# Kernel tuning notes

Hardware: AMD Instinct MI355X
Metric: run time of the kernel (lower is better)

## Reference

```python
import jax, jax.numpy as jnp
import numpy as np

N = 50000      # nodes
E = 800000     # edges (avg degree 16)
F_IN = 64      # node_feature_space
H = 64         # hidden_dim
G = 16         # graphs in batch
BN_EPS = 1e-5


def setup_inputs() -> dict:
    key = jax.random.key(0)
    ks = jax.random.split(key, 8)
    x = jax.random.normal(ks[0], (N, F_IN), jnp.float32)
    edge_index = jax.random.randint(ks[1], (2, E), 0, N, dtype=jnp.int64)
    batch = jnp.sort(jax.random.randint(ks[2], (N,), 0, G, dtype=jnp.int64))
    init = lambda k, shp, fan: jax.random.normal(k, shp, jnp.float32) / np.float32(np.sqrt(fan))
    params = dict(
        W1_0=init(ks[3], (F_IN, H), F_IN), b1_0=jnp.zeros((H,), jnp.float32),
        W2_0=init(ks[4], (H, H), H),       b2_0=jnp.zeros((H,), jnp.float32),
        g_0=jnp.ones((H,), jnp.float32),   be_0=jnp.zeros((H,), jnp.float32),
        W1_1=init(ks[5], (H, H), H),       b1_1=jnp.zeros((H,), jnp.float32),
        W2_1=init(ks[6], (H, H), H),       b2_1=jnp.zeros((H,), jnp.float32),
        g_1=jnp.ones((H,), jnp.float32),   be_1=jnp.zeros((H,), jnp.float32),
    )
    return dict(x=x, edge_index=edge_index, batch=batch, **params)


def _gin_layer(x, src, dst, W1, b1, W2, b2, g, be):
    # GINConv (eps=0): h_i = MLP(x_i + sum_{j->i} x_j)
    agg = jax.ops.segment_sum(x[src], dst, num_segments=N)   # [N, d]
    h = x + agg
    h = jnp.maximum(h @ W1 + b1, 0.0) @ W2 + b2              # Linear-ReLU-Linear
    # BatchNorm1d (training-mode batch stats, biased variance as in torch)
    mu = h.mean(axis=0)
    var = h.var(axis=0)
    h = (h - mu) * jax.lax.rsqrt(var + BN_EPS) * g + be
    return jnp.maximum(h, 0.0)                               # ReLU


def reference(x, edge_index, batch,
              W1_0, b1_0, W2_0, b2_0, g_0, be_0,
              W1_1, b1_1, W2_1, b2_1, g_1, be_1):
    src, dst = edge_index[0], edge_index[1]
    x = _gin_layer(x, src, dst, W1_0, b1_0, W2_0, b2_0, g_0, be_0)
    x = _gin_layer(x, src, dst, W1_1, b1_1, W2_1, b2_1, g_1, be_1)
    # global_mean_pool over graph ids
    cnt = jax.ops.segment_sum(jnp.ones((N,), x.dtype), batch, num_segments=G)
    sums = jax.ops.segment_sum(x, batch, num_segments=G)
    h_graph = sums / jnp.maximum(cnt, 1.0)[:, None]
    return (x, h_graph)
```

## Files before the change

kernel.cpp:

```cpp
#include <hip/hip_runtime.h>
#include <hip/hip_bf16.h>


constexpr int NN = 50000;
constexpr int NE = 800000;
constexpr int HD = 64;
constexpr int NG = 16;
constexpr float BN_EPS = 1e-5f;
constexpr int ROWCAP = 64;
constexpr int NPART = 8;
constexpr int PSZ = 6250;
constexpr int PBLK = (PSZ + 3) / 4;

__global__ __launch_bounds__(256)
void prep_kernel(const float* __restrict__ x, __hip_bfloat16* __restrict__ xb,
                 int* __restrict__ cnt, float* __restrict__ stats0,
                 float* __restrict__ stats1, float* __restrict__ psums) {
    int i4 = blockIdx.x * 256 + threadIdx.x;
    if (i4 < NN) cnt[i4] = 0;
    if (blockIdx.x == 0) {
        if (threadIdx.x < 128) stats0[threadIdx.x] = 0.f;
        else stats1[threadIdx.x - 128] = 0.f;
    } else if (blockIdx.x == 1) {
        *(float4*)(psums + threadIdx.x * 4) = make_float4(0.f, 0.f, 0.f, 0.f);
    }
    if (i4 >= NN * HD / 4) return;
    float4 v = *(const float4*)(x + (size_t)i4 * 4);
    union { ushort4 u; __hip_bfloat16 b[4]; } p;
    p.b[0] = __float2bfloat16(v.x);
    p.b[1] = __float2bfloat16(v.y);
    p.b[2] = __float2bfloat16(v.z);
    p.b[3] = __float2bfloat16(v.w);
    *(ushort4*)((unsigned short*)xb + (size_t)i4 * 4) = p.u;
}

__global__ __launch_bounds__(256)
void scatter_kernel(const int* __restrict__ ei, int* __restrict__ cnt,
                    unsigned short* __restrict__ csr) {
    int p = blockIdx.x & 7;
    int chunk = blockIdx.x >> 3;
    int e4 = (chunk * 256 + threadIdx.x) * 4;
    if (e4 >= NE) return;
    int4 s = *(const int4*)(ei + e4);
    int4 d = *(const int4*)(ei + NE + e4);
    int lo = p * PSZ, hi = lo + PSZ;
    int slot;
    if (d.x >= lo && d.x < hi) {
        slot = atomicAdd(&cnt[d.x], 1);
        if (slot < ROWCAP) csr[(d.x << 6) + slot] = (unsigned short)s.x;
    }
    if (d.y >= lo && d.y < hi) {
        slot = atomicAdd(&cnt[d.y], 1);
        if (slot < ROWCAP) csr[(d.y << 6) + slot] = (unsigned short)s.y;
    }
    if (d.z >= lo && d.z < hi) {
        slot = atomicAdd(&cnt[d.z], 1);
        if (slot < ROWCAP) csr[(d.z << 6) + slot] = (unsigned short)s.z;
    }
    if (d.w >= lo && d.w < hi) {
        slot = atomicAdd(&cnt[d.w], 1);
        if (slot < ROWCAP) csr[(d.w << 6) + slot] = (unsigned short)s.w;
    }
}

template <int MODE>
__global__ __launch_bounds__(256)
void agg_kernel(const float* __restrict__ xin, const __hip_bfloat16* __restrict__ xg,
                const int* __restrict__ cnt, const unsigned short* __restrict__ csr,
                const float* __restrict__ stats_prev, const float* __restrict__ gp,
                const float* __restrict__ bep, float* __restrict__ h) {
    int lr = ((blockIdx.x >> 3) << 2) + (threadIdx.x >> 6);
    if (lr >= PSZ) return;
    int row = (blockIdx.x & 7) * PSZ + lr;
    int lane = threadIdx.x & 63;
    int s4 = (lane & 15) * 4;
    int g = lane >> 4;

    float4 sc4 = make_float4(1.f, 1.f, 1.f, 1.f);
    float4 off4 = make_float4(0.f, 0.f, 0.f, 0.f);
    if (MODE == 1) {
        const float inv = 1.f / (float)NN;
        float4 sm = *(const float4*)(stats_prev + s4);
        float4 sq = *(const float4*)(stats_prev + 64 + s4);
        float4 gg = *(const float4*)(gp + s4);
        float4 bb = *(const float4*)(bep + s4);
        float mu, var;
        mu = sm.x * inv; var = sq.x * inv - mu * mu;
        sc4.x = gg.x * rsqrtf(var + BN_EPS); off4.x = bb.x - mu * sc4.x;
        mu = sm.y * inv; var = sq.y * inv - mu * mu;
        sc4.y = gg.y * rsqrtf(var + BN_EPS); off4.y = bb.y - mu * sc4.y;
        mu = sm.z * inv; var = sq.z * inv - mu * mu;
        sc4.z = gg.z * rsqrtf(var + BN_EPS); off4.z = bb.z - mu * sc4.z;
        mu = sm.w * inv; var = sq.w * inv - mu * mu;
        sc4.w = gg.w * rsqrtf(var + BN_EPS); off4.w = bb.w - mu * sc4.w;
    }

    int m = min(cnt[row], ROWCAP);
    int ids = (int)csr[((size_t)row << 6) + lane];
    const unsigned short* xgp = (const unsigned short*)xg;

    float4 accA = make_float4(0.f, 0.f, 0.f, 0.f);
    float4 accB = make_float4(0.f, 0.f, 0.f, 0.f);
    if (g == 0) {
        float4 sv = *(const float4*)(xin + (size_t)row * HD + s4);
        if (MODE == 1) {
            accA.x = fmaxf(fmaf(sv.x, sc4.x, off4.x), 0.f);
            accA.y = fmaxf(fmaf(sv.y, sc4.y, off4.y), 0.f);
            accA.z = fmaxf(fmaf(sv.z, sc4.z, off4.z), 0.f);
            accA.w = fmaxf(fmaf(sv.w, sc4.w, off4.w), 0.f);
        } else {
            accA = sv;
        }
    }

#define ACC_U2(ACC, U)                                                        \
    {                                                                         \
        float v0 = __uint_as_float((U).x << 16);                              \
        float v1 = __uint_as_float((U).x & 0xffff0000u);                      \
        float v2 = __uint_as_float((U).y << 16);                              \
        float v3 = __uint_as_float((U).y & 0xffff0000u);                      \
        if (MODE == 1) {                                                      \
            ACC.x += fmaxf(fmaf(v0, sc4.x, off4.x), 0.f);                     \
            ACC.y += fmaxf(fmaf(v1, sc4.y, off4.y), 0.f);                     \
            ACC.z += fmaxf(fmaf(v2, sc4.z, off4.z), 0.f);                     \
            ACC.w += fmaxf(fmaf(v3, sc4.w, off4.w), 0.f);                     \
        } else {                                                              \
            ACC.x += v0; ACC.y += v1; ACC.z += v2; ACC.w += v3;               \
        }                                                                     \
    }

    int j = 0;
    for (; j + 8 <= m; j += 8) {
        int nb0 = __shfl(ids, j + g);
        int nb1 = __shfl(ids, j + 4 + g);
        uint2 u0 = *(const uint2*)(xgp + ((size_t)nb0 << 6) + s4);
        uint2 u1 = *(const uint2*)(xgp + ((size_t)nb1 << 6) + s4);
        ACC_U2(accA, u0);
        ACC_U2(accB, u1);
    }
    for (; j < m; j += 4) {
        int nb = __shfl(ids, j + g);
        if (j + g < m) {
            uint2 u = *(const uint2*)(xgp + ((size_t)nb << 6) + s4);
            ACC_U2(accA, u);
        }
    }
#undef ACC_U2

    float4 acc = make_float4(accA.x + accB.x, accA.y + accB.y,
                             accA.z + accB.z, accA.w + accB.w);
    acc.x += __shfl_xor(acc.x, 16);
    acc.y += __shfl_xor(acc.y, 16);
    acc.z += __shfl_xor(acc.z, 16);
    acc.w += __shfl_xor(acc.w, 16);
    acc.x += __shfl_xor(acc.x, 32);
    acc.y += __shfl_xor(acc.y, 32);
    acc.z += __shfl_xor(acc.z, 32);
    acc.w += __shfl_xor(acc.w, 32);

    if (g == 0)
        *(float4*)(h + (size_t)row * HD + s4) = acc;
}

__global__ __launch_bounds__(256)
void mlp_kernel(const float* __restrict__ hin, float* __restrict__ hout,
                const float* __restrict__ W1, const float* __restrict__ b1,
                const float* __restrict__ W2, const float* __restrict__ b2,
                float* __restrict__ stats, __hip_bfloat16* __restrict__ xbr) {
    __shared__ float sh[128 * 65];
    __shared__ float sW[64 * 64];
    __shared__ float sb[64];
    __shared__ float red[2][4][64];
    int tid = threadIdx.x;
    int base = blockIdx.x * 128;

    for (int i = tid; i < 4096; i += 256) sW[i] = W1[i];
    if (tid < 64) sb[tid] = b1[tid];
#pragma unroll
    for (int i = 0; i < 8; i++) {
        int i4 = tid + 256 * i;
        int row = i4 >> 4, col = (i4 & 15) * 4;
        int grow = base + row;
        float4 v = (grow < NN) ? *(const float4*)(hin + (size_t)grow * HD + col)
                               : make_float4(0.f, 0.f, 0.f, 0.f);
        float* d = sh + row * 65 + col;
        d[0] = v.x; d[1] = v.y; d[2] = v.z; d[3] = v.w;
    }
    __syncthreads();

    int wv = tid >> 6;
    int lane = tid & 63;

    float acc0[16], acc1[16];
#pragma unroll
    for (int j = 0; j < 16; j++) { acc0[j] = sb[wv * 16 + j]; acc1[j] = acc0[j]; }
    for (int k = 0; k < 64; k++) {
        float a0 = sh[lane * 65 + k];
        float a1 = sh[(64 + lane) * 65 + k];
        const float4* wr = (const float4*)(sW + k * 64 + wv * 16);
#pragma unroll
        for (int q = 0; q < 4; q++) {
            float4 w = wr[q];
            acc0[4 * q + 0] = fmaf(a0, w.x, acc0[4 * q + 0]);
            acc0[4 * q + 1] = fmaf(a0, w.y, acc0[4 * q + 1]);
            acc0[4 * q + 2] = fmaf(a0, w.z, acc0[4 * q + 2]);
            acc0[4 * q + 3] = fmaf(a0, w.w, acc0[4 * q + 3]);
            acc1[4 * q + 0] = fmaf(a1, w.x, acc1[4 * q + 0]);
            acc1[4 * q + 1] = fmaf(a1, w.y, acc1[4 * q + 1]);
            acc1[4 * q + 2] = fmaf(a1, w.z, acc1[4 * q + 2]);
            acc1[4 * q + 3] = fmaf(a1, w.w, acc1[4 * q + 3]);
        }
    }
    __syncthreads();

#pragma unroll
    for (int j = 0; j < 16; j++) {
        sh[lane * 65 + wv * 16 + j] = fmaxf(acc0[j], 0.f);
        sh[(64 + lane) * 65 + wv * 16 + j] = fmaxf(acc1[j], 0.f);
    }
    for (int i = tid; i < 4096; i += 256) sW[i] = W2[i];
    if (tid < 64) sb[tid] = b2[tid];
    __syncthreads();

#pragma unroll
    for (int j = 0; j < 16; j++) { acc0[j] = sb[wv * 16 + j]; acc1[j] = acc0[j]; }
    for (int k = 0; k < 64; k++) {
        float a0 = sh[lane * 65 + k];
        float a1 = sh[(64 + lane) * 65 + k];
        const float4* wr = (const float4*)(sW + k * 64 + wv * 16);
#pragma unroll
        for (int q = 0; q < 4; q++) {
            float4 w = wr[q];
            acc0[4 * q + 0] = fmaf(a0, w.x, acc0[4 * q + 0]);
            acc0[4 * q + 1] = fmaf(a0, w.y, acc0[4 * q + 1]);
            acc0[4 * q + 2] = fmaf(a0, w.z, acc0[4 * q + 2]);
            acc0[4 * q + 3] = fmaf(a0, w.w, acc0[4 * q + 3]);
            acc1[4 * q + 0] = fmaf(a1, w.x, acc1[4 * q + 0]);
            acc1[4 * q + 1] = fmaf(a1, w.y, acc1[4 * q + 1]);
            acc1[4 * q + 2] = fmaf(a1, w.z, acc1[4 * q + 2]);
            acc1[4 * q + 3] = fmaf(a1, w.w, acc1[4 * q + 3]);
        }
    }
    __syncthreads();
#pragma unroll
    for (int j = 0; j < 16; j++) {
        sh[lane * 65 + wv * 16 + j] = acc0[j];
        sh[(64 + lane) * 65 + wv * 16 + j] = acc1[j];
    }
    __syncthreads();

#pragma unroll
    for (int i = 0; i < 8; i++) {
        int i4 = tid + 256 * i;
        int row = i4 >> 4, col = (i4 & 15) * 4;
        int grow = base + row;
        if (grow < NN) {
            const float* s = sh + row * 65 + col;
            float4 v = make_float4(s[0], s[1], s[2], s[3]);
            *(float4*)(hout + (size_t)grow * HD + col) = v;
            if (xbr) {
                union { ushort4 u; __hip_bfloat16 b[4]; } p;
                p.b[0] = __float2bfloat16(v.x);
                p.b[1] = __float2bfloat16(v.y);
                p.b[2] = __float2bfloat16(v.z);
                p.b[3] = __float2bfloat16(v.w);
                *(ushort4*)((unsigned short*)xbr + (size_t)grow * HD + col) = p.u;
            }
        }
    }

    {
        int col = tid & 63;
        int r0 = (tid >> 6) * 32;
        float s = 0.f, ss = 0.f;
#pragma unroll
        for (int r = 0; r < 32; r++) {
            float v = (base + r0 + r < NN) ? sh[(r0 + r) * 65 + col] : 0.f;
            s += v;
            ss += v * v;
        }
        red[0][tid >> 6][col] = s;
        red[1][tid >> 6][col] = ss;
        __syncthreads();
        if (tid < 64) {
            float S = red[0][0][col] + red[0][1][col] + red[0][2][col] + red[0][3][col];
            atomicAdd(stats + col, S);
        } else if (tid < 128) {
            float SS = red[1][0][col] + red[1][1][col] + red[1][2][col] + red[1][3][col];
            atomicAdd(stats + 64 + col, SS);
        }
    }
}

__global__ __launch_bounds__(256)
void norm_kernel(float* h, const float* __restrict__ stats,
                 const float* __restrict__ g, const float* __restrict__ be,
                 const int* __restrict__ batch, float* __restrict__ psums) {
    __shared__ float sg[2][64];
    if (threadIdx.x < 128) sg[threadIdx.x >> 6][threadIdx.x & 63] = 0.f;
    __syncthreads();
    size_t i4 = (size_t)blockIdx.x * 256 + threadIdx.x;
    int row = (int)(i4 >> 4);
    int base_row = blockIdx.x * 16;
    int g0 = batch[base_row];
    size_t off = i4 * 4;
    int col = (int)(off & 63);
    float4 v = *(const float4*)(h + off);
    float4 sm = *(const float4*)(stats + col);
    float4 sq = *(const float4*)(stats + 64 + col);
    float4 gg = *(const float4*)(g + col);
    float4 bb = *(const float4*)(be + col);
    const float inv = 1.f / (float)NN;
    float4 o;
    {
        float mu = sm.x * inv, var = sq.x * inv - mu * mu;
        float sc = gg.x * rsqrtf(var + BN_EPS);
        o.x = fmaxf((v.x - mu) * sc + bb.x, 0.f);
    }
    {
        float mu = sm.y * inv, var = sq.y * inv - mu * mu;
        float sc = gg.y * rsqrtf(var + BN_EPS);
        o.y = fmaxf((v.y - mu) * sc + bb.y, 0.f);
    }
    {
        float mu = sm.z * inv, var = sq.z * inv - mu * mu;
        float sc = gg.z * rsqrtf(var + BN_EPS);
        o.z = fmaxf((v.z - mu) * sc + bb.z, 0.f);
    }
    {
        float mu = sm.w * inv, var = sq.w * inv - mu * mu;
        float sc = gg.w * rsqrtf(var + BN_EPS);
        o.w = fmaxf((v.w - mu) * sc + bb.w, 0.f);
    }
    *(float4*)(h + off) = o;

    int dg = batch[row] - g0;
    if (dg <= 1) {
        atomicAdd(&sg[dg][col + 0], o.x);
        atomicAdd(&sg[dg][col + 1], o.y);
        atomicAdd(&sg[dg][col + 2], o.z);
        atomicAdd(&sg[dg][col + 3], o.w);
    } else {
        int gid = g0 + dg;
        atomicAdd(&psums[gid * HD + col + 0], o.x);
        atomicAdd(&psums[gid * HD + col + 1], o.y);
        atomicAdd(&psums[gid * HD + col + 2], o.z);
        atomicAdd(&psums[gid * HD + col + 3], o.w);
    }
    __syncthreads();
    if (threadIdx.x < 128) {
        int d = threadIdx.x >> 6;
        int c = threadIdx.x & 63;
        float s = sg[d][c];
        if (g0 + d < NG && s != 0.f) atomicAdd(&psums[(g0 + d) * HD + c], s);
    }
}

__device__ __forceinline__ int lower_bound_batch(const int* __restrict__ b, int val) {
    int lo = 0, hi = NN;
    while (lo < hi) {
        int mid = (lo + hi) >> 1;
        if (b[mid] < val) lo = mid + 1;
        else hi = mid;
    }
    return lo;
}

__global__ __launch_bounds__(1024)
void pool_finalize_kernel(const float* __restrict__ sums, const int* __restrict__ batch,
                          float* __restrict__ out) {
    int g = threadIdx.x >> 6;
    int col = threadIdx.x & 63;
    int s = lower_bound_batch(batch, g);
    int e = lower_bound_batch(batch, g + 1);
    float cnt = (float)(e - s);
    out[g * HD + col] = sums[g * HD + col] / fmaxf(cnt, 1.f);
}

extern "C" void kernel_launch(void* const* d_in, const int* in_sizes, int n_in,
                              void* d_out, int out_size, void* d_ws, size_t ws_size,
                              hipStream_t stream) {
    const float* x = (const float*)d_in[0];
    const int* ei = (const int*)d_in[1];
    const int* batch = (const int*)d_in[2];
    const float* W1_0 = (const float*)d_in[3];
    const float* b1_0 = (const float*)d_in[4];
    const float* W2_0 = (const float*)d_in[5];
    const float* b2_0 = (const float*)d_in[6];
    const float* g_0 = (const float*)d_in[7];
    const float* be_0 = (const float*)d_in[8];
    const float* W1_1 = (const float*)d_in[9];
    const float* b1_1 = (const float*)d_in[10];
    const float* W2_1 = (const float*)d_in[11];
    const float* b2_1 = (const float*)d_in[12];
    const float* g_1 = (const float*)d_in[13];
    const float* be_1 = (const float*)d_in[14];

    float* out = (float*)d_out;

    float* buf_h = (float*)d_ws;
    float* stats0 = buf_h + (size_t)NN * HD;
    float* stats1 = stats0 + 128;
    float* psums = stats1 + 128;
    int* cnt = (int*)(psums + 1024);
    unsigned short* csr = (unsigned short*)(cnt + NN);
    __hip_bfloat16* xb = (__hip_bfloat16*)(csr + (size_t)NN * ROWCAP);

    dim3 b256(256);
    int mlp_grid = (NN + 127) / 128;
    int norm_grid = (NN * HD / 4 + 255) / 256;
    int sct_grid = ((NE + 1023) / 1024) * NPART;
    int agg_grid = NPART * PBLK;

    prep_kernel<<<norm_grid, b256, 0, stream>>>(x, xb, cnt, stats0, stats1, psums);
    scatter_kernel<<<sct_grid, b256, 0, stream>>>(ei, cnt, csr);

    agg_kernel<0><<<agg_grid, b256, 0, stream>>>(x, xb, cnt, csr,
                                                 nullptr, nullptr, nullptr, buf_h);
    mlp_kernel<<<mlp_grid, b256, 0, stream>>>(buf_h, out, W1_0, b1_0, W2_0, b2_0,
                                              stats0, xb);

    agg_kernel<1><<<agg_grid, b256, 0, stream>>>(out, xb, cnt, csr,
                                                 stats0, g_0, be_0, buf_h);
    mlp_kernel<<<mlp_grid, b256, 0, stream>>>(buf_h, out, W1_1, b1_1, W2_1, b2_1,
                                              stats1, (__hip_bfloat16*)nullptr);

    norm_kernel<<<norm_grid, b256, 0, stream>>>(out, stats1, g_1, be_1, batch, psums);
    pool_finalize_kernel<<<1, dim3(1024), 0, stream>>>(psums, batch, out + (size_t)NN * HD);
}
```

Before: 273.1 us.

## Split aggregation feature columns across two block halves with 8 neighbors per wave step

The aggregation kernel now launches twice as many blocks, and each half of the grid handles 32 of the 64 feature columns. Each wave processes 8 neighbors at once with 8 lanes per neighbor instead of 4 neighbors with 16 lanes each. This gives more memory-level parallelism per wave and more blocks to hide gather latency. In exchange, each 64-byte row segment is split into two 32-byte pieces fetched by different blocks, and the csr/count reads and an extra shuffle-reduction stage are duplicated.

```diff
diff --git a/kernel.cpp b/kernel.cpp
--- a/kernel.cpp
+++ b/kernel.cpp
@@ -11,6 +11,7 @@
 constexpr int NPART = 8;
 constexpr int PSZ = 6250;
 constexpr int PBLK = (PSZ + 3) / 4;
+constexpr int HBLK = NPART * PBLK;
 
 __global__ __launch_bounds__(256)
 void prep_kernel(const float* __restrict__ x, __hip_bfloat16* __restrict__ xb,
@@ -69,21 +70,25 @@
                 const int* __restrict__ cnt, const unsigned short* __restrict__ csr,
                 const float* __restrict__ stats_prev, const float* __restrict__ gp,
                 const float* __restrict__ bep, float* __restrict__ h) {
-    int lr = ((blockIdx.x >> 3) << 2) + (threadIdx.x >> 6);
+    int b = blockIdx.x;
+    int hh = (b >= HBLK) ? 1 : 0;
+    int b2 = b - hh * HBLK;
+    int lr = ((b2 >> 3) << 2) + (threadIdx.x >> 6);
     if (lr >= PSZ) return;
-    int row = (blockIdx.x & 7) * PSZ + lr;
+    int row = (b2 & 7) * PSZ + lr;
     int lane = threadIdx.x & 63;
-    int s4 = (lane & 15) * 4;
-    int g = lane >> 4;
+    int s = lane & 7;
+    int g = lane >> 3;
+    int c0 = hh * 32 + s * 4;
 
     float4 sc4 = make_float4(1.f, 1.f, 1.f, 1.f);
     float4 off4 = make_float4(0.f, 0.f, 0.f, 0.f);
     if (MODE == 1) {
         const float inv = 1.f / (float)NN;
-        float4 sm = *(const float4*)(stats_prev + s4);
-        float4 sq = *(const float4*)(stats_prev + 64 + s4);
-        float4 gg = *(const float4*)(gp + s4);
-        float4 bb = *(const float4*)(bep + s4);
+        float4 sm = *(const float4*)(stats_prev + c0);
+        float4 sq = *(const float4*)(stats_prev + 64 + c0);
+        float4 gg = *(const float4*)(gp + c0);
+        float4 bb = *(const float4*)(bep + c0);
         float mu, var;
         mu = sm.x * inv; var = sq.x * inv - mu * mu;
         sc4.x = gg.x * rsqrtf(var + BN_EPS); off4.x = bb.x - mu * sc4.x;
@@ -102,7 +107,7 @@
     float4 accA = make_float4(0.f, 0.f, 0.f, 0.f);
     float4 accB = make_float4(0.f, 0.f, 0.f, 0.f);
     if (g == 0) {
-        float4 sv = *(const float4*)(xin + (size_t)row * HD + s4);
+        float4 sv = *(const float4*)(xin + (size_t)row * HD + c0);
         if (MODE == 1) {
             accA.x = fmaxf(fmaf(sv.x, sc4.x, off4.x), 0.f);
             accA.y = fmaxf(fmaf(sv.y, sc4.y, off4.y), 0.f);
@@ -130,18 +135,18 @@
     }
 
     int j = 0;
-    for (; j + 8 <= m; j += 8) {
+    for (; j + 16 <= m; j += 16) {
         int nb0 = __shfl(ids, j + g);
-        int nb1 = __shfl(ids, j + 4 + g);
-        uint2 u0 = *(const uint2*)(xgp + ((size_t)nb0 << 6) + s4);
-        uint2 u1 = *(const uint2*)(xgp + ((size_t)nb1 << 6) + s4);
+        int nb1 = __shfl(ids, j + 8 + g);
+        uint2 u0 = *(const uint2*)(xgp + ((size_t)nb0 << 6) + c0);
+        uint2 u1 = *(const uint2*)(xgp + ((size_t)nb1 << 6) + c0);
         ACC_U2(accA, u0);
         ACC_U2(accB, u1);
     }
-    for (; j < m; j += 4) {
+    for (; j < m; j += 8) {
         int nb = __shfl(ids, j + g);
         if (j + g < m) {
-            uint2 u = *(const uint2*)(xgp + ((size_t)nb << 6) + s4);
+            uint2 u = *(const uint2*)(xgp + ((size_t)nb << 6) + c0);
             ACC_U2(accA, u);
         }
     }
@@ -149,6 +154,10 @@
 
     float4 acc = make_float4(accA.x + accB.x, accA.y + accB.y,
                              accA.z + accB.z, accA.w + accB.w);
+    acc.x += __shfl_xor(acc.x, 8);
+    acc.y += __shfl_xor(acc.y, 8);
+    acc.z += __shfl_xor(acc.z, 8);
+    acc.w += __shfl_xor(acc.w, 8);
     acc.x += __shfl_xor(acc.x, 16);
     acc.y += __shfl_xor(acc.y, 16);
     acc.z += __shfl_xor(acc.z, 16);
@@ -159,7 +168,7 @@
     acc.w += __shfl_xor(acc.w, 32);
 
     if (g == 0)
-        *(float4*)(h + (size_t)row * HD + s4) = acc;
+        *(float4*)(h + (size_t)row * HD + c0) = acc;
 }
 
 __global__ __launch_bounds__(256)
@@ -410,7 +419,7 @@
     int mlp_grid = (NN + 127) / 128;
     int norm_grid = (NN * HD / 4 + 255) / 256;
     int sct_grid = ((NE + 1023) / 1024) * NPART;
-    int agg_grid = NPART * PBLK;
+    int agg_grid = 2 * HBLK;
 
     prep_kernel<<<norm_grid, b256, 0, stream>>>(x, xb, cnt, stats0, stats1, psums);
     scatter_kernel<<<sct_grid, b256, 0, stream>>>(ei, cnt, csr);
```

Result: slower. 289.6 us (+6.0%).
